# Kernel tuning notes

Hardware: AMD Instinct MI355X
Metric: run time of the kernel (lower is better)

## Reference

```python
import jax, jax.numpy as jnp
import numpy as np

NUM_GRAPHS = 128


def _gcn_conv(x, W, b, src, dst, norm, n_nodes):
    # PyG GCNConv: linear transform, then symmetric-normalized scatter-add aggregation
    h = x @ W                                  # [N, out]
    msg = norm[:, None] * h[src]               # [E+N, out] gathered messages
    out = jax.ops.segment_sum(msg, dst, num_segments=n_nodes)
    return out + b


def setup_inputs() -> dict:
    key = jax.random.key(0)
    ks = jax.random.split(key, 12)
    N, E, H, GE, C = 100000, 1000000, 64, 64, 5
    x = jax.random.normal(ks[0], (N, 2), dtype=jnp.float32)
    edge_index = jax.random.randint(ks[1], (2, E), 0, N, dtype=jnp.int32)
    batch = jnp.sort(jax.random.randint(ks[2], (N,), 0, NUM_GRAPHS, dtype=jnp.int32))
    graph_embedding = jax.random.normal(ks[3], (NUM_GRAPHS, GE), dtype=jnp.float32)
    s = lambda k, shape, fan: jax.random.normal(k, shape, dtype=jnp.float32) * (1.0 / np.sqrt(fan))
    W1 = s(ks[4], (2, H), 2); b1 = jnp.zeros((H,), jnp.float32)
    W2 = s(ks[5], (H, H), H); b2 = jnp.zeros((H,), jnp.float32)
    W3 = s(ks[6], (H, H), H); b3 = jnp.zeros((H,), jnp.float32)
    Wl = s(ks[7], (H + GE, C), H + GE); bl = jnp.zeros((C,), jnp.float32)
    return {"x": x, "edge_index": edge_index, "batch": batch,
            "graph_embedding": graph_embedding,
            "W1": W1, "b1": b1, "W2": W2, "b2": b2, "W3": W3, "b3": b3,
            "Wl": Wl, "bl": bl}


def reference(x, edge_index, batch, graph_embedding, W1, b1, W2, b2, W3, b3, Wl, bl):
    N = x.shape[0]
    loops = jnp.arange(N, dtype=edge_index.dtype)
    src = jnp.concatenate([edge_index[0], loops])   # add self-loops
    dst = jnp.concatenate([edge_index[1], loops])
    deg = jax.ops.segment_sum(jnp.ones_like(dst, dtype=x.dtype), dst, num_segments=N)
    dinv = jnp.where(deg > 0, jax.lax.rsqrt(deg), 0.0)
    norm = dinv[src] * dinv[dst]                    # [E+N]

    h = jax.nn.relu(_gcn_conv(x, W1, b1, src, dst, norm, N))
    h = jax.nn.relu(_gcn_conv(h, W2, b2, src, dst, norm, N))
    h = _gcn_conv(h, W3, b3, src, dst, norm, N)

    # global mean pool over graphs
    sums = jax.ops.segment_sum(h, batch, num_segments=NUM_GRAPHS)
    cnts = jax.ops.segment_sum(jnp.ones((N,), x.dtype), batch, num_segments=NUM_GRAPHS)
    pooled = sums / jnp.maximum(cnts, 1.0)[:, None]

    z = jnp.concatenate([pooled, graph_embedding], axis=1) @ Wl + bl
    return jax.nn.log_softmax(z, axis=1)
```

## Files before the change

kernel.cpp:

```cpp
#include <hip/hip_runtime.h>
#include <hip/hip_bf16.h>
#include <math.h>

#define NG 128
#define CHUNKB 2048
#define NBIN 512
#define EWIN 256
#define STAGE_CAP 6144

typedef __attribute__((ext_vector_type(8))) short short8;
typedef __attribute__((ext_vector_type(4))) float float4v;
typedef __attribute__((ext_vector_type(4))) uint uint4v;

__global__ void k_bin_hist(const int* __restrict__ dst, int* __restrict__ hist,
                           int e, int nb, float* __restrict__ sums,
                           const float* __restrict__ W2, const float* __restrict__ W3,
                           __hip_bfloat16* __restrict__ Wf2, __hip_bfloat16* __restrict__ Wf3) {
    __shared__ int h[NBIN];
    int blk = blockIdx.x;
    if (blk >= nb) {
        int ex = blk - nb;
        if (ex == 0) {
            for (int i = threadIdx.x; i < NG * 64; i += 256) sums[i] = 0.0f;
        } else {
            const float* W = (ex == 2) ? W3 : W2;
            __hip_bfloat16* Wf = (ex == 2) ? Wf3 : Wf2;
            for (int t = threadIdx.x; t < 512; t += 256) {
                int c = t >> 6, l = t & 63;
                int jt = c >> 1, half = c & 1, nn = l & 15, q = l >> 4;
                #pragma unroll
                for (int j = 0; j < 8; j++) {
                    int k = half * 32 + q * 8 + j;
                    Wf[t * 8 + j] = __float2bfloat16(W[k * 64 + jt * 16 + nn]);
                }
            }
        }
        return;
    }
    for (int i = threadIdx.x; i < NBIN; i += 256) h[i] = 0;
    __syncthreads();
    int base = blk * CHUNKB;
    int lim = e - base; if (lim > CHUNKB) lim = CHUNKB;
    for (int k = threadIdx.x; k < lim; k += 256)
        atomicAdd(&h[dst[base + k] >> 8], 1);
    __syncthreads();
    for (int b = threadIdx.x; b < NBIN; b += 256) hist[b * nb + blk] = h[b];
}

__global__ void __launch_bounds__(512) genscan1(int* __restrict__ a, int* __restrict__ bsums, int n) {
    __shared__ int s[512];
    int tid = threadIdx.x;
    int i = blockIdx.x * 512 + tid;
    int v = (i < n) ? a[i] : 0;
    s[tid] = v;
    __syncthreads();
    for (int d = 1; d < 512; d <<= 1) {
        int t = (tid >= d) ? s[tid - d] : 0;
        __syncthreads();
        s[tid] += t;
        __syncthreads();
    }
    if (i < n) a[i] = s[tid] - v;
    if (tid == 511) bsums[blockIdx.x] = s[511];
}

__global__ void __launch_bounds__(512) genscan2(int* __restrict__ bsums, int nb) {
    __shared__ int s[512];
    int tid = threadIdx.x;
    int v = (tid < nb) ? bsums[tid] : 0;
    s[tid] = v;
    __syncthreads();
    for (int d = 1; d < 512; d <<= 1) {
        int t = (tid >= d) ? s[tid - d] : 0;
        __syncthreads();
        s[tid] += t;
        __syncthreads();
    }
    if (tid < nb) bsums[tid] = s[tid] - v;
}

__global__ void k_bin_scatter(const int* __restrict__ srcs, const int* __restrict__ dsts,
                              const int* __restrict__ offsets, const int* __restrict__ bsums,
                              int* __restrict__ outbuf, int e, int nb) {
    __shared__ int hcnt[NBIN];
    __shared__ int lstart[NBIN];
    __shared__ int ss[256];
    __shared__ int stage[CHUNKB];
    __shared__ int sbuck[CHUNKB];
    int tid = threadIdx.x, blk = blockIdx.x, base = blk * CHUNKB;
    int lim = e - base; if (lim > CHUNKB) lim = CHUNKB;
    for (int i = tid; i < NBIN; i += 256) hcnt[i] = 0;
    __syncthreads();
    for (int k = tid; k < lim; k += 256)
        atomicAdd(&hcnt[dsts[base + k] >> 8], 1);
    __syncthreads();
    int c0 = hcnt[2 * tid], c1 = hcnt[2 * tid + 1];
    int sum = c0 + c1;
    ss[tid] = sum;
    __syncthreads();
    for (int d = 1; d < 256; d <<= 1) {
        int t = (tid >= d) ? ss[tid - d] : 0;
        __syncthreads();
        ss[tid] += t;
        __syncthreads();
    }
    int excl = ss[tid] - sum;
    lstart[2 * tid] = excl;
    lstart[2 * tid + 1] = excl + c0;
    __syncthreads();
    hcnt[2 * tid] = excl;
    hcnt[2 * tid + 1] = excl + c0;
    __syncthreads();
    for (int k = tid; k < lim; k += 256) {
        int s = srcs[base + k], d = dsts[base + k];
        int bk = d >> 8;
        int p = atomicAdd(&hcnt[bk], 1);
        stage[p] = ((d & 255) << 24) | s;
        sbuck[p] = bk;
    }
    __syncthreads();
    for (int i = tid; i < NBIN; i += 256) {
        int gi = i * nb + blk;
        lstart[i] = offsets[gi] + bsums[gi >> 9] - lstart[i];
    }
    __syncthreads();
    for (int p = tid; p < lim; p += 256)
        outbuf[lstart[sbuck[p]] + p] = stage[p];
}

__global__ void k_csrAB(const int* __restrict__ ebuck, const int* __restrict__ offsets,
                        const int* __restrict__ bsums, const float* __restrict__ x,
                        int* __restrict__ row_ptr, float* __restrict__ dinv,
                        float2* __restrict__ xs, int* __restrict__ csr,
                        int n, int nb, int e_total) {
    __shared__ int lcnt[256];
    __shared__ int ssc[256];
    __shared__ int rstart[256];
    __shared__ int stage[STAGE_CAP];
    int b = blockIdx.x, tid = threadIdx.x, n0 = b << 8;
    lcnt[tid] = 0;
    __syncthreads();
    int i0 = b * nb, i1 = (b + 1) * nb;
    int e0 = offsets[i0] + bsums[i0 >> 9];
    int e1 = offsets[i1] + bsums[i1 >> 9];
    int cnt = e1 - e0;
    bool fast = (cnt <= STAGE_CAP);
    if (fast) {
        for (int i = e0 + tid; i < e1; i += 256) {
            int p = ebuck[i];
            stage[i - e0] = p;
            atomicAdd(&lcnt[(uint)p >> 24], 1);
        }
    } else {
        for (int i = e0 + tid; i < e1; i += 256)
            atomicAdd(&lcnt[(uint)ebuck[i] >> 24], 1);
    }
    __syncthreads();
    int v = lcnt[tid];
    ssc[tid] = v;
    __syncthreads();
    for (int d = 1; d < 256; d <<= 1) {
        int t = (tid >= d) ? ssc[tid - d] : 0;
        __syncthreads();
        ssc[tid] += t;
        __syncthreads();
    }
    int rs = e0 + ssc[tid] - v;
    rstart[tid] = rs;
    int node = n0 + tid;
    if (node < n) {
        row_ptr[node] = rs;
        float dv = rsqrtf((float)v + 1.0f);
        dinv[node] = dv;
        const float2* x2 = (const float2*)x;
        float2 xi = x2[node];
        xs[node] = make_float2(xi.x * dv, xi.y * dv);
        if (node == n - 1) row_ptr[n] = e_total;
    }
    lcnt[tid] = 0;
    __syncthreads();
    if (fast) {
        for (int i = tid; i < cnt; i += 256) {
            int p = stage[i];
            int li = (uint)p >> 24;
            int r = atomicAdd(&lcnt[li], 1);
            csr[rstart[li] + r] = p & 0xFFFFFF;
        }
    } else {
        for (int i = e0 + tid; i < e1; i += 256) {
            int p = ebuck[i];
            int li = (uint)p >> 24;
            int r = atomicAdd(&lcnt[li], 1);
            csr[rstart[li] + r] = p & 0xFFFFFF;
        }
    }
}

__global__ void k_layer1(const int* __restrict__ row_ptr, const int* __restrict__ edges,
                         const float2* __restrict__ xs, const float* __restrict__ dinv,
                         const float* __restrict__ W1, const float* __restrict__ b1,
                         __hip_bfloat16* __restrict__ h, int n) {
    __shared__ float w1s[128];
    __shared__ float b1s[64];
    if (threadIdx.x < 128) w1s[threadIdx.x] = W1[threadIdx.x];
    if (threadIdx.x < 64) b1s[threadIdx.x] = b1[threadIdx.x];
    __syncthreads();
    int i = blockIdx.x * blockDim.x + threadIdx.x;
    if (i >= n) return;
    float dd = dinv[i];
    float2 xi = xs[i];
    float a0 = xi.x, a1 = xi.y;
    int lo = row_ptr[i], hi = row_ptr[i + 1];
    int k = lo;
    for (; k + 4 <= hi; k += 4) {
        int s0 = edges[k], s1 = edges[k + 1], s2 = edges[k + 2], s3 = edges[k + 3];
        float2 v0 = xs[s0], v1 = xs[s1], v2 = xs[s2], v3 = xs[s3];
        a0 += v0.x + v1.x + v2.x + v3.x;
        a1 += v0.y + v1.y + v2.y + v3.y;
    }
    for (; k < hi; k++) {
        float2 v = xs[edges[k]];
        a0 += v.x;
        a1 += v.y;
    }
    a0 *= dd; a1 *= dd;
    short8* hv = reinterpret_cast<short8*>(h + (size_t)i * 64);
    #pragma unroll
    for (int g = 0; g < 8; g++) {
        short8 pack;
        #pragma unroll
        for (int j = 0; j < 8; j++) {
            int col = g * 8 + j;
            float v = fmaxf(a0 * w1s[col] + a1 * w1s[64 + col] + b1s[col], 0.0f);
            v *= dd;
            __hip_bfloat16 bv = __float2bfloat16(v);
            pack[j] = *reinterpret_cast<short*>(&bv);
        }
        hv[g] = pack;
    }
}

static __device__ __forceinline__ void acc8(float* a, uint4v v) {
    #pragma unroll
    for (int i = 0; i < 4; i++) {
        uint u = v[i];
        a[2 * i]     += __int_as_float(u << 16);
        a[2 * i + 1] += __int_as_float(u & 0xffff0000u);
    }
}

template <bool FAST>
static __device__ __forceinline__ void agg_group(int lo, int cnt, int mc, int c,
        const int* __restrict__ gE, const int* EW, int wave_lo,
        const uint4v* __restrict__ hin4, float* acc) {
    for (int j = 0; j < mc; j += 4) {
        bool ok0 = j < cnt, ok1 = j + 1 < cnt, ok2 = j + 2 < cnt, ok3 = j + 3 < cnt;
        int e0 = ok0 ? lo + j     : wave_lo;
        int e1 = ok1 ? lo + j + 1 : wave_lo;
        int e2 = ok2 ? lo + j + 2 : wave_lo;
        int e3 = ok3 ? lo + j + 3 : wave_lo;
        int s0 = FAST ? EW[e0 - wave_lo] : gE[e0];
        int s1 = FAST ? EW[e1 - wave_lo] : gE[e1];
        int s2 = FAST ? EW[e2 - wave_lo] : gE[e2];
        int s3 = FAST ? EW[e3 - wave_lo] : gE[e3];
        uint4v v0 = hin4[(size_t)s0 * 8 + c];
        uint4v v1 = hin4[(size_t)s1 * 8 + c];
        uint4v v2 = hin4[(size_t)s2 * 8 + c];
        uint4v v3 = hin4[(size_t)s3 * 8 + c];
        if (!ok0) v0 = (uint4v){0u, 0u, 0u, 0u};
        if (!ok1) v1 = (uint4v){0u, 0u, 0u, 0u};
        if (!ok2) v2 = (uint4v){0u, 0u, 0u, 0u};
        if (!ok3) v3 = (uint4v){0u, 0u, 0u, 0u};
        acc8(acc, v0);
        acc8(acc, v1);
        acc8(acc, v2);
        acc8(acc, v3);
    }
}

template <int RELU, int POOL>
__global__ void __launch_bounds__(64, 8) k_aggLin(const int* __restrict__ row_ptr,
                                                  const int* __restrict__ edges,
                                                  const __hip_bfloat16* __restrict__ hin,
                                                  const float* __restrict__ dinv,
                                                  const __hip_bfloat16* __restrict__ Wf,
                                                  const float* __restrict__ b,
                                                  __hip_bfloat16* __restrict__ hout,
                                                  const int* __restrict__ batch,
                                                  float* __restrict__ sums, int n) {
    __shared__ __attribute__((aligned(16))) __hip_bfloat16 T[16 * 72];
    __shared__ int EW[EWIN];
    int lane = threadIdx.x;
    int nb0 = blockIdx.x * 16;
    if (nb0 >= n) return;
    int g = lane >> 3;
    int c = lane & 7;
    const uint4v* hin4 = reinterpret_cast<const uint4v*>(hin);

    int bidx = nb0 + (lane < 16 ? lane : 16);
    if (bidx > n) bidx = n;
    int rp = row_ptr[bidx];
    int wave_lo = __shfl(rp, 0);
    int wave_hi = __shfl(rp, 16);
    int cnt_all = wave_hi - wave_lo;
    bool fast = (cnt_all <= EWIN);
    if (fast)
        for (int i = lane; i < cnt_all; i += 64) EW[i] = edges[wave_lo + i];

    #pragma unroll
    for (int h8 = 0; h8 < 2; h8++) {
        int nn = h8 * 8 + g;
        int node = nb0 + nn;
        float acc[8] = {0.f, 0.f, 0.f, 0.f, 0.f, 0.f, 0.f, 0.f};
        int lo = __shfl(rp, nn);
        int hi = __shfl(rp, nn + 1);
        int cnt = (node < n) ? (hi - lo) : 0;
        int mc = cnt;
        mc = max(mc, __shfl_xor(mc, 8));
        mc = max(mc, __shfl_xor(mc, 16));
        mc = max(mc, __shfl_xor(mc, 32));
        if (node < n)
            acc8(acc, hin4[(size_t)node * 8 + c]);
        if (fast) agg_group<true >(lo, cnt, mc, c, edges, EW, wave_lo, hin4, acc);
        else      agg_group<false>(lo, cnt, mc, c, edges, EW, wave_lo, hin4, acc);
        float dv = (node < n) ? dinv[node] : 0.0f;
        uint4v pk;
        #pragma unroll
        for (int i = 0; i < 4; i++) {
            __hip_bfloat16 bx = __float2bfloat16(acc[2 * i] * dv);
            __hip_bfloat16 by = __float2bfloat16(acc[2 * i + 1] * dv);
            pk[i] = (uint)(*reinterpret_cast<unsigned short*>(&bx)) |
                    ((uint)(*reinterpret_cast<unsigned short*>(&by)) << 16);
        }
        *reinterpret_cast<uint4v*>(&T[nn * 72 + c * 8]) = pk;
    }

    int m = lane & 15, q = lane >> 4;
    short8 a0 = *reinterpret_cast<const short8*>(&T[m * 72 + q * 8]);
    short8 a1 = *reinterpret_cast<const short8*>(&T[m * 72 + 32 + q * 8]);
    int lastn = nb0 + 15 < n ? nb0 + 15 : n - 1;
    bool onegraph = POOL && (nb0 + 15 < n) && (batch[nb0] == batch[lastn]);
    int gA = POOL ? batch[nb0] : 0;
    float dvs[4];
    if (!POOL) {
        #pragma unroll
        for (int r = 0; r < 4; r++) {
            int node = nb0 + q * 4 + r;
            dvs[r] = node < n ? dinv[node] : 0.0f;
        }
    }
    #pragma unroll
    for (int jt = 0; jt < 4; jt++) {
        short8 bf0 = *reinterpret_cast<const short8*>(Wf + ((size_t)(jt * 2 + 0) * 64 + lane) * 8);
        short8 bf1 = *reinterpret_cast<const short8*>(Wf + ((size_t)(jt * 2 + 1) * 64 + lane) * 8);
        float4v d = {0.0f, 0.0f, 0.0f, 0.0f};
        d = __builtin_amdgcn_mfma_f32_16x16x32_bf16(a0, bf0, d, 0, 0, 0);
        d = __builtin_amdgcn_mfma_f32_16x16x32_bf16(a1, bf1, d, 0, 0, 0);
        float bias = b[jt * 16 + m];
        if (POOL) {
            if (onegraph) {
                float s = (d[0] + bias) + (d[1] + bias) + (d[2] + bias) + (d[3] + bias);
                s += __shfl_xor(s, 16);
                s += __shfl_xor(s, 32);
                if (q == 0) atomicAdd(&sums[gA * 64 + jt * 16 + m], s);
            } else {
                #pragma unroll
                for (int r = 0; r < 4; r++) {
                    int node = nb0 + q * 4 + r;
                    if (node < n)
                        atomicAdd(&sums[batch[node] * 64 + jt * 16 + m], d[r] + bias);
                }
            }
        } else {
            #pragma unroll
            for (int r = 0; r < 4; r++) {
                int node = nb0 + q * 4 + r;
                if (node < n) {
                    float v = d[r] + bias;
                    if (RELU) v = fmaxf(v, 0.0f);
                    v *= dvs[r];
                    hout[(size_t)node * 64 + jt * 16 + m] = __float2bfloat16(v);
                }
            }
        }
    }
}

__device__ inline int lower_bound_i(const int* __restrict__ a, int n, int key) {
    int lo = 0, hi = n;
    while (lo < hi) {
        int mid = (lo + hi) >> 1;
        if (a[mid] < key) lo = mid + 1; else hi = mid;
    }
    return lo;
}

__global__ void k_head(const float* __restrict__ sums, const int* __restrict__ batch,
                       const float* __restrict__ ge, const float* __restrict__ Wl,
                       const float* __restrict__ bl, float* __restrict__ out,
                       int n, int ng) {
    int g = blockIdx.x * blockDim.x + threadIdx.x;
    if (g < ng) {
        int lo = lower_bound_i(batch, n, g);
        int hi = lower_bound_i(batch, n, g + 1);
        float c = fmaxf((float)(hi - lo), 1.0f);
        float z[5];
        for (int cl = 0; cl < 5; cl++) z[cl] = bl[cl];
        for (int k = 0; k < 64; k++) {
            float p = sums[g * 64 + k] / c;
            for (int cl = 0; cl < 5; cl++) z[cl] += p * Wl[k * 5 + cl];
        }
        for (int k = 0; k < 64; k++) {
            float p = ge[g * 64 + k];
            for (int cl = 0; cl < 5; cl++) z[cl] += p * Wl[(64 + k) * 5 + cl];
        }
        float m = z[0];
        for (int cl = 1; cl < 5; cl++) m = fmaxf(m, z[cl]);
        float s = 0.0f;
        for (int cl = 0; cl < 5; cl++) s += expf(z[cl] - m);
        float lse = m + logf(s);
        for (int cl = 0; cl < 5; cl++) out[g * 5 + cl] = z[cl] - lse;
    }
}

#define ALIGN16(x) (((x) + 15) & ~(size_t)15)

extern "C" void kernel_launch(void* const* d_in, const int* in_sizes, int n_in,
                              void* d_out, int out_size, void* d_ws, size_t ws_size,
                              hipStream_t stream) {
    const float* x    = (const float*)d_in[0];
    const int*   ei   = (const int*)d_in[1];
    const int*   batch= (const int*)d_in[2];
    const float* ge   = (const float*)d_in[3];
    const float* W1   = (const float*)d_in[4];
    const float* b1   = (const float*)d_in[5];
    const float* W2   = (const float*)d_in[6];
    const float* b2   = (const float*)d_in[7];
    const float* W3   = (const float*)d_in[8];
    const float* b3   = (const float*)d_in[9];
    const float* Wl   = (const float*)d_in[10];
    const float* bl   = (const float*)d_in[11];
    float* out = (float*)d_out;

    const int N = in_sizes[0] / 2;
    const int E = in_sizes[1] / 2;
    const int* src = ei;
    const int* dst = ei + E;
    const int NBUK = (N + 255) >> 8;
    const int nbC  = (E + CHUNKB - 1) / CHUNKB;

    char* wsb = (char*)d_ws;
    float* dinv   = (float*)wsb;                wsb += ALIGN16((size_t)N * 4);
    float2* xs    = (float2*)wsb;               wsb += ALIGN16((size_t)N * 8);
    __hip_bfloat16* h16 = (__hip_bfloat16*)wsb;  wsb += ALIGN16((size_t)64 * N * 2);
    __hip_bfloat16* buf2= (__hip_bfloat16*)wsb;  wsb += ALIGN16((size_t)64 * N * 2);
    float* sums   = (float*)wsb;                wsb += ALIGN16((size_t)NG * 64 * 4);
    __hip_bfloat16* Wf2 = (__hip_bfloat16*)wsb; wsb += ALIGN16((size_t)4096 * 2);
    __hip_bfloat16* Wf3 = (__hip_bfloat16*)wsb; wsb += ALIGN16((size_t)4096 * 2);
    int*   ebuck  = (int*)wsb;                  wsb += ALIGN16((size_t)E * 4);
    int*   csr    = (int*)wsb;                  wsb += ALIGN16((size_t)E * 4);
    int*   row_ptr= (int*)wsb;                  wsb += ALIGN16((size_t)(N + 1) * 4);
    int*   hist   = (int*)wsb;                  wsb += ALIGN16((size_t)NBIN * nbC * 4);
    int*   bsums  = (int*)wsb;                  wsb += 512 * 4;

    const int BS = 256;
    int gN   = (N + BS - 1) / BS;
    int gF   = (N + 15) / 16;
    int nH   = NBIN * nbC;
    int gH   = (nH + 511) / 512;

    k_bin_hist<<<nbC + 3, BS, 0, stream>>>(dst, hist, E, nbC, sums, W2, W3, Wf2, Wf3);
    genscan1<<<gH, 512, 0, stream>>>(hist, bsums, nH);
    genscan2<<<1, 512, 0, stream>>>(bsums, gH);
    k_bin_scatter<<<nbC, BS, 0, stream>>>(src, dst, hist, bsums, ebuck, E, nbC);
    k_csrAB<<<NBUK, BS, 0, stream>>>(ebuck, hist, bsums, x, row_ptr, dinv, xs, csr,
                                     N, nbC, E);

    k_layer1<<<gN, BS, 0, stream>>>(row_ptr, csr, xs, dinv, W1, b1, h16, N);

    k_aggLin<1, 0><<<gF, 64, 0, stream>>>(row_ptr, csr, h16, dinv, Wf2, b2, buf2,
                                          nullptr, nullptr, N);

    k_aggLin<0, 1><<<gF, 64, 0, stream>>>(row_ptr, csr, buf2, dinv, Wf3, b3, nullptr,
                                          batch, sums, N);

    k_head<<<1, 128, 0, stream>>>(sums, batch, ge, Wl, bl, out, N, NG);
}
```

Measured before the change: 198.3 us.

## Partition CSR neighbor lists by source range and aggregate in phases

During CSR build, each node's neighbor list is sub-sorted into four source-index ranges, and the per-range counts are packed as bytes into a new bcnt array. The aggregation kernels then walk the neighbors phase by phase, so all waves gather from roughly the same quarter of the feature table at once, which is meant to improve L2/MALL locality of the random gathers. The cost is extra shared atomics and a divide during CSR construction, plus per-phase max reductions and less ILP within each group's loop. The packed 8-bit counts would overflow if a node had more than 255 in-edges from one range.

```diff
diff --git a/kernel.cpp b/kernel.cpp
--- a/kernel.cpp
+++ b/kernel.cpp
@@ -7,6 +7,7 @@
 #define NBIN 512
 #define EWIN 256
 #define STAGE_CAP 6144
+#define NPH 4
 
 typedef __attribute__((ext_vector_type(8))) short short8;
 typedef __attribute__((ext_vector_type(4))) float float4v;
@@ -132,13 +133,17 @@
                         const int* __restrict__ bsums, const float* __restrict__ x,
                         int* __restrict__ row_ptr, float* __restrict__ dinv,
                         float2* __restrict__ xs, int* __restrict__ csr,
-                        int n, int nb, int e_total) {
+                        uint* __restrict__ bcnt, int n, int nb, int e_total, int qb) {
     __shared__ int lcnt[256];
     __shared__ int ssc[256];
     __shared__ int rstart[256];
+    __shared__ int l8[256 * NPH];
+    __shared__ int p8[256 * NPH];
     __shared__ int stage[STAGE_CAP];
     int b = blockIdx.x, tid = threadIdx.x, n0 = b << 8;
     lcnt[tid] = 0;
+    #pragma unroll
+    for (int k = 0; k < NPH; k++) l8[tid * NPH + k] = 0;
     __syncthreads();
     int i0 = b * nb, i1 = (b + 1) * nb;
     int e0 = offsets[i0] + bsums[i0 >> 9];
@@ -149,11 +154,17 @@
         for (int i = e0 + tid; i < e1; i += 256) {
             int p = ebuck[i];
             stage[i - e0] = p;
-            atomicAdd(&lcnt[(uint)p >> 24], 1);
+            int li = (uint)p >> 24, sb = (p & 0xFFFFFF) / qb;
+            atomicAdd(&lcnt[li], 1);
+            atomicAdd(&l8[li * NPH + sb], 1);
         }
     } else {
-        for (int i = e0 + tid; i < e1; i += 256)
-            atomicAdd(&lcnt[(uint)ebuck[i] >> 24], 1);
+        for (int i = e0 + tid; i < e1; i += 256) {
+            int p = ebuck[i];
+            int li = (uint)p >> 24, sb = (p & 0xFFFFFF) / qb;
+            atomicAdd(&lcnt[li], 1);
+            atomicAdd(&l8[li * NPH + sb], 1);
+        }
     }
     __syncthreads();
     int v = lcnt[tid];
@@ -168,7 +179,14 @@
     int rs = e0 + ssc[tid] - v;
     rstart[tid] = rs;
     int node = n0 + tid;
+    int c0 = l8[tid * NPH + 0], c1 = l8[tid * NPH + 1];
+    int c2 = l8[tid * NPH + 2], c3 = l8[tid * NPH + 3];
+    p8[tid * NPH + 0] = 0;
+    p8[tid * NPH + 1] = c0;
+    p8[tid * NPH + 2] = c0 + c1;
+    p8[tid * NPH + 3] = c0 + c1 + c2;
     if (node < n) {
+        bcnt[node] = (uint)c0 | ((uint)c1 << 8) | ((uint)c2 << 16) | ((uint)c3 << 24);
         row_ptr[node] = rs;
         float dv = rsqrtf((float)v + 1.0f);
         dinv[node] = dv;
@@ -177,21 +195,22 @@
         xs[node] = make_float2(xi.x * dv, xi.y * dv);
         if (node == n - 1) row_ptr[n] = e_total;
     }
-    lcnt[tid] = 0;
+    #pragma unroll
+    for (int k = 0; k < NPH; k++) l8[tid * NPH + k] = 0;
     __syncthreads();
     if (fast) {
         for (int i = tid; i < cnt; i += 256) {
             int p = stage[i];
-            int li = (uint)p >> 24;
-            int r = atomicAdd(&lcnt[li], 1);
-            csr[rstart[li] + r] = p & 0xFFFFFF;
+            int li = (uint)p >> 24, src = p & 0xFFFFFF, sb = src / qb;
+            int r = atomicAdd(&l8[li * NPH + sb], 1);
+            csr[rstart[li] + p8[li * NPH + sb] + r] = src;
         }
     } else {
         for (int i = e0 + tid; i < e1; i += 256) {
             int p = ebuck[i];
-            int li = (uint)p >> 24;
-            int r = atomicAdd(&lcnt[li], 1);
-            csr[rstart[li] + r] = p & 0xFFFFFF;
+            int li = (uint)p >> 24, src = p & 0xFFFFFF, sb = src / qb;
+            int r = atomicAdd(&l8[li * NPH + sb], 1);
+            csr[rstart[li] + p8[li * NPH + sb] + r] = src;
         }
     }
 }
@@ -287,7 +306,8 @@
                                                   const float* __restrict__ b,
                                                   __hip_bfloat16* __restrict__ hout,
                                                   const int* __restrict__ batch,
-                                                  float* __restrict__ sums, int n) {
+                                                  float* __restrict__ sums,
+                                                  const uint* __restrict__ bcnt, int n) {
     __shared__ __attribute__((aligned(16))) __hip_bfloat16 T[16 * 72];
     __shared__ int EW[EWIN];
     int lane = threadIdx.x;
@@ -300,6 +320,7 @@
     int bidx = nb0 + (lane < 16 ? lane : 16);
     if (bidx > n) bidx = n;
     int rp = row_ptr[bidx];
+    uint c32v = (lane < 16 && bidx < n) ? bcnt[bidx] : 0u;
     int wave_lo = __shfl(rp, 0);
     int wave_hi = __shfl(rp, 16);
     int cnt_all = wave_hi - wave_lo;
@@ -313,16 +334,24 @@
         int node = nb0 + nn;
         float acc[8] = {0.f, 0.f, 0.f, 0.f, 0.f, 0.f, 0.f, 0.f};
         int lo = __shfl(rp, nn);
-        int hi = __shfl(rp, nn + 1);
-        int cnt = (node < n) ? (hi - lo) : 0;
-        int mc = cnt;
-        mc = max(mc, __shfl_xor(mc, 8));
-        mc = max(mc, __shfl_xor(mc, 16));
-        mc = max(mc, __shfl_xor(mc, 32));
+        uint c32 = __shfl((int)c32v, nn);
         if (node < n)
             acc8(acc, hin4[(size_t)node * 8 + c]);
-        if (fast) agg_group<true >(lo, cnt, mc, c, edges, EW, wave_lo, hin4, acc);
-        else      agg_group<false>(lo, cnt, mc, c, edges, EW, wave_lo, hin4, acc);
+        int off = 0;
+        #pragma unroll
+        for (int ph = 0; ph < NPH; ph++) {
+            int cp = (int)((c32 >> (8 * ph)) & 255u);
+            int lop = lo + off;
+            off += cp;
+            int mc = cp;
+            mc = max(mc, __shfl_xor(mc, 8));
+            mc = max(mc, __shfl_xor(mc, 16));
+            mc = max(mc, __shfl_xor(mc, 32));
+            if (mc > 0) {
+                if (fast) agg_group<true >(lop, cp, mc, c, edges, EW, wave_lo, hin4, acc);
+                else      agg_group<false>(lop, cp, mc, c, edges, EW, wave_lo, hin4, acc);
+            }
+        }
         float dv = (node < n) ? dinv[node] : 0.0f;
         uint4v pk;
         #pragma unroll
@@ -448,6 +477,7 @@
     const int* dst = ei + E;
     const int NBUK = (N + 255) >> 8;
     const int nbC  = (E + CHUNKB - 1) / CHUNKB;
+    const int QB   = (N + NPH - 1) / NPH;
 
     char* wsb = (char*)d_ws;
     float* dinv   = (float*)wsb;                wsb += ALIGN16((size_t)N * 4);
@@ -460,6 +490,7 @@
     int*   ebuck  = (int*)wsb;                  wsb += ALIGN16((size_t)E * 4);
     int*   csr    = (int*)wsb;                  wsb += ALIGN16((size_t)E * 4);
     int*   row_ptr= (int*)wsb;                  wsb += ALIGN16((size_t)(N + 1) * 4);
+    uint*  bcnt   = (uint*)wsb;                 wsb += ALIGN16((size_t)N * 4);
     int*   hist   = (int*)wsb;                  wsb += ALIGN16((size_t)NBIN * nbC * 4);
     int*   bsums  = (int*)wsb;                  wsb += 512 * 4;
 
@@ -474,15 +505,15 @@
     genscan2<<<1, 512, 0, stream>>>(bsums, gH);
     k_bin_scatter<<<nbC, BS, 0, stream>>>(src, dst, hist, bsums, ebuck, E, nbC);
     k_csrAB<<<NBUK, BS, 0, stream>>>(ebuck, hist, bsums, x, row_ptr, dinv, xs, csr,
-                                     N, nbC, E);
+                                     bcnt, N, nbC, E, QB);
 
     k_layer1<<<gN, BS, 0, stream>>>(row_ptr, csr, xs, dinv, W1, b1, h16, N);
 
     k_aggLin<1, 0><<<gF, 64, 0, stream>>>(row_ptr, csr, h16, dinv, Wf2, b2, buf2,
-                                          nullptr, nullptr, N);
+                                          nullptr, nullptr, bcnt, N);
 
     k_aggLin<0, 1><<<gF, 64, 0, stream>>>(row_ptr, csr, buf2, dinv, Wf3, b3, nullptr,
-                                          batch, sums, N);
+                                          batch, sums, bcnt, N);
 
     k_head<<<1, 128, 0, stream>>>(sums, batch, ge, Wl, bl, out, N, NG);
 }
```

Result: slower. 205.9 us (+3.8%).
